# Optimization experiments

Hardware: AMD Instinct MI355X
Metric: run time of the kernel (lower is better)

Reference implementation:

```python
import jax, jax.numpy as jnp
import numpy as np

N_HEADS = 32
N_KV_HEADS = 8
HEAD_DIM = 64
D_MODEL = 2048
SLIDING_WINDOW = 512
ROPE_THETA = 10000.0
PAST_LENGTH = 0
EPS = 1e-6


def setup_inputs() -> dict:
    key = jax.random.key(0)
    k1, k2, k3 = jax.random.split(key, 3)
    B, S = 1, 2048
    q_size = N_HEADS * HEAD_DIM
    kv_size = N_KV_HEADS * HEAD_DIM
    return {
        "x": jax.random.normal(k1, (B, S, D_MODEL), dtype=jnp.float32),
        "w_qkv": jax.random.normal(k2, (q_size + 2 * kv_size, D_MODEL), dtype=jnp.float32) * (D_MODEL ** -0.5),
        "w_out": jax.random.normal(k3, (D_MODEL, q_size), dtype=jnp.float32) * (q_size ** -0.5),
        "q_norm_w": jnp.ones((HEAD_DIM,), dtype=jnp.float32),
        "k_norm_w": jnp.ones((HEAD_DIM,), dtype=jnp.float32),
    }


def _rms_norm(x, w):
    xf = x.astype(jnp.float32)
    rms = jax.lax.rsqrt(jnp.mean(xf * xf, axis=-1, keepdims=True) + EPS)
    return (xf * rms).astype(x.dtype) * w


def _rope(q, k, past_length):
    # q: [b, h, s, d], k: [b, kv, s, d]
    s, d = q.shape[2], q.shape[3]
    inv_freq = 1.0 / (ROPE_THETA ** (jnp.arange(0, d, 2, dtype=jnp.float32) / d))
    pos = jnp.arange(s, dtype=jnp.float32) + past_length
    ang = pos[:, None] * inv_freq[None, :]            # [s, d/2]
    emb = jnp.concatenate([ang, ang], axis=-1)        # [s, d]
    cos, sin = jnp.cos(emb), jnp.sin(emb)

    def rot_half(x):
        x1, x2 = jnp.split(x, 2, axis=-1)
        return jnp.concatenate([-x2, x1], axis=-1)

    q = q * cos + rot_half(q) * sin
    k = k * cos + rot_half(k) * sin
    return q, k


def _sliding_mask(seq_len, total_len, past_length):
    q_idx = jnp.arange(seq_len)[:, None]
    k_idx = jnp.arange(total_len)[None, :]
    causal = (q_idx + past_length) >= k_idx
    window = (q_idx + past_length - k_idx) < SLIDING_WINDOW
    keep = causal & window
    return jnp.where(keep, 0.0, -jnp.inf).astype(jnp.float32)[None, None]


def reference(x, w_qkv, w_out, q_norm_w, k_norm_w):
    b, s, _ = x.shape
    n_rep = N_HEADS // N_KV_HEADS
    q_size = N_HEADS * HEAD_DIM
    kv_size = N_KV_HEADS * HEAD_DIM

    qkv = jnp.einsum('bsd,od->bso', x, w_qkv)
    q, k, v = jnp.split(qkv, [q_size, q_size + kv_size], axis=-1)
    q = q.reshape(b, s, N_HEADS, HEAD_DIM).transpose(0, 2, 1, 3)
    k = k.reshape(b, s, N_KV_HEADS, HEAD_DIM).transpose(0, 2, 1, 3)
    v = v.reshape(b, s, N_KV_HEADS, HEAD_DIM).transpose(0, 2, 1, 3)

    q = _rms_norm(q, q_norm_w)
    k = _rms_norm(k, k_norm_w)
    q, k = _rope(q, k, PAST_LENGTH)

    k_rep = jnp.repeat(k, n_rep, axis=1)  # [b, H, s, d]
    v_rep = jnp.repeat(v, n_rep, axis=1)

    scale = HEAD_DIM ** -0.5
    scores = jnp.einsum('bhqd,bhkd->bhqk', q, k_rep) * scale
    scores = scores + _sliding_mask(s, s, PAST_LENGTH)
    probs = jax.nn.softmax(scores, axis=-1)
    attn = jnp.einsum('bhqk,bhkd->bhqd', probs, v_rep)

    attn = attn.transpose(0, 2, 1, 3).reshape(b, s, q_size)
    return jnp.einsum('bso,do->bsd', attn, w_out)
```

## Files before the change

### kernel.cpp

```cpp
#include <hip/hip_runtime.h>

typedef unsigned short u16;
typedef unsigned int u32;
typedef __bf16 bf16x8 __attribute__((ext_vector_type(8)));
typedef float f32x4 __attribute__((ext_vector_type(4)));
typedef float f32x16 __attribute__((ext_vector_type(16)));
typedef u16 u16x8 __attribute__((ext_vector_type(8)));
typedef u32 u32x2 __attribute__((ext_vector_type(2)));
typedef u32 u32x4 __attribute__((ext_vector_type(4)));

#define MFMA16(a, b, c) __builtin_amdgcn_mfma_f32_16x16x32_bf16((a), (b), (c), 0, 0, 0)
#define MFMA32(a, b, c) __builtin_amdgcn_mfma_f32_32x32x16_bf16((a), (b), (c), 0, 0, 0)

__device__ __forceinline__ u16 f2bf(float f) {
    unsigned int u = __float_as_uint(f);
    u = (u + 0x7FFF + ((u >> 16) & 1)) >> 16;
    return (u16)u;
}

__device__ __forceinline__ u32 cvtpk(float a, float b) {
    u32 d;
    asm("v_cvt_pk_bf16_f32 %0, %1, %2" : "=v"(d) : "v"(a), "v"(b));
    return d;
}

__device__ __forceinline__ void gld_lds16(const u16* g, u16* l) {
    __builtin_amdgcn_global_load_lds(
        (const __attribute__((address_space(1))) unsigned int*)g,
        (__attribute__((address_space(3))) unsigned int*)l, 16, 0, 0);
}

__global__ __launch_bounds__(256) void cvt_bf16(const float* __restrict__ in,
                                                u16* __restrict__ out, int n4) {
    int idx = blockIdx.x * blockDim.x + threadIdx.x;
    int stride = gridDim.x * blockDim.x;
    for (int i = idx; i < n4; i += stride) {
        float4 v = reinterpret_cast<const float4*>(in)[i];
        ushort4 o;
        o.x = f2bf(v.x); o.y = f2bf(v.y); o.z = f2bf(v.z); o.w = f2bf(v.w);
        reinterpret_cast<ushort4*>(out)[i] = o;
    }
}

__global__ __launch_bounds__(256) void reduce_add(const float4* __restrict__ a,
                                                  const float4* __restrict__ b,
                                                  float4* __restrict__ o, int n4) {
    int idx = blockIdx.x * blockDim.x + threadIdx.x;
    int stride = gridDim.x * blockDim.x;
    for (int i = idx; i < n4; i += stride) {
        float4 va = a[i], vb = b[i];
        float4 vo = {va.x + vb.x, va.y + vb.y, va.z + vb.z, va.w + vb.w};
        o[i] = vo;
    }
}

template <int SPLITK, int RM, int RN, int XN>
__global__ __launch_bounds__(256) void gemm_bt(const u16* __restrict__ A,
                                               const u16* __restrict__ B,
                                               float* __restrict__ C,
                                               int M, int N, int K) {
    __shared__ __align__(16) u16 As[3][128 * 32];
    __shared__ __align__(16) u16 Bs[3][128 * 32];

    int bid = blockIdx.x;
    int xcd = bid & 7;
    int r = bid >> 3;
    int tm = (xcd / XN) * RM + (r / RN);
    int tn = (xcd % XN) * RN + (r % RN);
    int m0 = tm << 7, n0 = tn << 7;

    int Ks = K / SPLITK;
    int kbase = blockIdx.y * Ks;
    float* Cs = C + (size_t)blockIdx.y * ((size_t)M * N);

    int t = threadIdx.x;
    int w = t >> 6, l = t & 63, lrow = l & 15, lhi = l >> 4;
    int wr = w >> 1, wc = w & 1;

    int e0 = t * 8;
    int row0 = t >> 2;
    int col0 = (((t & 3) ^ ((t >> 3) & 3)) << 3);

    const u16* Ag = A + (size_t)m0 * K + kbase;
    const u16* Bg = B + (size_t)n0 * K + kbase;

    auto stage = [&](int sbuf, int kt) {
        int k0 = kt << 5;
        gld_lds16(Ag + (size_t)row0 * K + k0 + col0, &As[sbuf][e0]);
        gld_lds16(Ag + (size_t)(row0 + 64) * K + k0 + col0, &As[sbuf][e0 + 2048]);
        gld_lds16(Bg + (size_t)row0 * K + k0 + col0, &Bs[sbuf][e0]);
        gld_lds16(Bg + (size_t)(row0 + 64) * K + k0 + col0, &Bs[sbuf][e0 + 2048]);
    };

    f32x4 acc[4][4] = {};
    int NT = Ks >> 5;
    stage(0, 0); stage(1, 1); stage(2, 2);
    asm volatile("s_waitcnt vmcnt(8)" ::: "memory");
    asm volatile("s_barrier" ::: "memory");
    int cur = 0;
    for (int kt = 0; kt < NT; ++kt) {
        bf16x8 af[4], bfr[4];
#pragma unroll
        for (int i = 0; i < 4; ++i) {
            int row = wr * 64 + i * 16 + lrow;
            af[i] = *(const bf16x8*)&As[cur][row * 32 + ((lhi ^ ((row >> 1) & 3)) << 3)];
        }
#pragma unroll
        for (int j = 0; j < 4; ++j) {
            int row = wc * 64 + j * 16 + lrow;
            bfr[j] = *(const bf16x8*)&Bs[cur][row * 32 + ((lhi ^ ((row >> 1) & 3)) << 3)];
        }
        asm volatile("s_waitcnt lgkmcnt(0)" ::: "memory");
        __builtin_amdgcn_sched_barrier(0);
        asm volatile("s_barrier" ::: "memory");
        if (kt + 3 < NT) stage(cur, kt + 3);
#pragma unroll
        for (int i = 0; i < 4; ++i)
#pragma unroll
            for (int j = 0; j < 4; ++j)
                acc[i][j] = MFMA16(af[i], bfr[j], acc[i][j]);
        if (kt + 1 < NT) {
            if (kt + 3 < NT)      asm volatile("s_waitcnt vmcnt(8)" ::: "memory");
            else if (kt + 2 < NT) asm volatile("s_waitcnt vmcnt(4)" ::: "memory");
            else                  asm volatile("s_waitcnt vmcnt(0)" ::: "memory");
            asm volatile("s_barrier" ::: "memory");
        }
        cur = (cur == 2) ? 0 : cur + 1;
    }
#pragma unroll
    for (int i = 0; i < 4; ++i) {
#pragma unroll
        for (int j = 0; j < 4; ++j) {
            int crow = m0 + wr * 64 + i * 16 + lhi * 4;
            int ccol = n0 + wc * 64 + j * 16 + lrow;
            float* cp = Cs + (size_t)crow * N + ccol;
#pragma unroll
            for (int r2 = 0; r2 < 4; ++r2) cp[(size_t)r2 * N] = acc[i][j][r2];
        }
    }
}

__global__ __launch_bounds__(256) void qkv_post(const float* __restrict__ qkv0,
                                                const float* __restrict__ qkv1,
                                                const float* __restrict__ qw,
                                                const float* __restrict__ kw,
                                                u16* __restrict__ qb,
                                                u16* __restrict__ kb,
                                                u16* __restrict__ vb) {
    const float C = 0.18033688011112042f;
    int s = blockIdx.x;
    int t = threadIdx.x, w = t >> 6, lane = t & 63;
    const float* row0 = qkv0 + (size_t)s * 3072;
    const float* row1 = qkv1 + (size_t)s * 3072;
    int d2 = lane & 31;
    float inv = exp2f(-(float)d2 * (13.287712379549449f / 32.0f));
    float ang = (float)s * inv;
    float cs = cosf(ang), sn = sinf(ang);
    for (int h = w; h < 48; h += 4) {
        float v = row0[h * 64 + lane] + row1[h * 64 + lane];
        if (h < 40) {
            float ss = v * v;
#pragma unroll
            for (int m = 32; m; m >>= 1) ss += __shfl_xor(ss, m);
            float rms = rsqrtf(ss * (1.0f / 64.0f) + 1e-6f);
            float wgt = (h < 32) ? qw[lane] : kw[lane];
            v = v * rms * wgt;
            float part = __shfl_xor(v, 32);
            float rot = (lane < 32) ? -part : part;
            v = v * cs + rot * sn;
            if (h < 32)
                qb[((size_t)h * 2048 + s) * 64 + lane] = f2bf(v * C);
            else
                kb[((size_t)(h - 32) * 2048 + s) * 64 + lane] = f2bf(v);
        } else {
            vb[((size_t)(h - 40) * 2048 + s) * 64 + lane] = f2bf(v);
        }
    }
}

__global__ __launch_bounds__(256) void transpose_v(const u16* __restrict__ vb,
                                                   u16* __restrict__ vt) {
    int kv = blockIdx.y;
    int s0 = blockIdx.x * 256;
    __shared__ __align__(16) u16 tile[64][256];
    int t = threadIdx.x;
    int sl = t >> 3;
    int d0 = (t & 7) * 8;
#pragma unroll
    for (int j = 0; j < 8; ++j) {
        int s = sl + j * 32;
        u16x8 v = *(const u16x8*)(vb + ((size_t)kv * 2048 + s0 + s) * 64 + d0);
#pragma unroll
        for (int e = 0; e < 8; ++e) tile[d0 + e][s] = v[e];
    }
    __syncthreads();
    int d = t >> 2;
    int so = (t & 3) * 64;
#pragma unroll
    for (int j = 0; j < 8; ++j) {
        int s_local = so + j * 8;
        *(u16x8*)(vt + ((size_t)kv * 64 + d) * 2048 + s0 + s_local) =
            *(const u16x8*)&tile[d][s_local];
    }
}

__global__ __launch_bounds__(256) void attn_fa7(const u16* __restrict__ qb,
                                                const u16* __restrict__ kb,
                                                const u16* __restrict__ vt,
                                                u16* __restrict__ ab) {
    int qt = blockIdx.x, h = blockIdx.y, kv = h >> 2;
    int t = threadIdx.x, w = t >> 6, l = t & 63;
    int lq = l & 31, hi = l >> 5;
    int qlo_blk = qt * 128;
    int qlo = qlo_blk + w * 32;
    __shared__ __align__(16) u16 Kt[2][32 * 64];
    __shared__ __align__(16) u16 Vt[2][64 * 32];
    __shared__ u16 sm[4][32][66];

    const u16* qrow = qb + ((size_t)h * 2048 + qlo + lq) * 64 + hi * 8;
    bf16x8 qf[4];
#pragma unroll
    for (int dk = 0; dk < 4; ++dk) qf[dk] = *(const bf16x8*)(qrow + dk * 16);

    f32x16 oa = {}, ob = {};
    float lsum = 0.f;

    int ktA = (qlo_blk >= 512) ? ((qlo_blk >> 5) - 16) : 0;
    int ktB = (qlo_blk >> 5) + 3;
    const u16* kb_h = kb + (size_t)kv * 2048 * 64;
    const u16* vt_h = vt + (size_t)kv * 64 * 2048;

    int sk_row = t >> 3, sk_c = ((t & 7) ^ (sk_row & 7)) << 3;
    int sv_row = t >> 2, sv_c = (((t & 3) ^ ((t >> 3) & 3))) << 3;

    auto stage = [&](int buf, int kt) {
        int k0 = kt << 5;
        gld_lds16(kb_h + (size_t)(k0 + sk_row) * 64 + sk_c, &Kt[buf][t * 8]);
        gld_lds16(vt_h + (size_t)sv_row * 2048 + k0 + sv_c, &Vt[buf][t * 8]);
    };

    stage(0, ktA);
    int cur = 0;
    for (int kt = ktA; kt <= ktB; ++kt) {
        if (kt < ktB) {
            stage(cur ^ 1, kt + 1);
            asm volatile("s_waitcnt vmcnt(2)" ::: "memory");
        } else {
            asm volatile("s_waitcnt vmcnt(0)" ::: "memory");
        }
        asm volatile("s_barrier" ::: "memory");

        int k0 = kt << 5;
        bool active = (k0 <= qlo + 31) && (k0 >= qlo - 542);
        if (active) {
            bf16x8 kf[4], vaf[2], vbf[2];
#pragma unroll
            for (int c = 0; c < 4; ++c)
                kf[c] = *(const bf16x8*)&Kt[cur][lq * 64 + (((c * 2 + hi) ^ (lq & 7)) << 3)];
#pragma unroll
            for (int vi = 0; vi < 2; ++vi) {
                int swz = ((vi * 2 + hi) ^ ((lq >> 1) & 3)) << 3;
                vaf[vi] = *(const bf16x8*)&Vt[cur][lq * 32 + swz];
                vbf[vi] = *(const bf16x8*)&Vt[cur][(lq + 32) * 32 + swz];
            }
            asm volatile("s_waitcnt lgkmcnt(0)" ::: "memory");
            __builtin_amdgcn_sched_barrier(0);

            f32x16 s = {};
            s = MFMA32(kf[0], qf[0], s);
            s = MFMA32(kf[1], qf[1], s);
            s = MFMA32(kf[2], qf[2], s);
            s = MFMA32(kf[3], qf[3], s);

            bool edge = (k0 + 31 > qlo) || (qlo + 31 - k0 >= 512);
            if (edge) {
                int q = qlo + lq;
#pragma unroll
                for (int r = 0; r < 16; ++r) {
                    int k = k0 + (r & 3) + 8 * (r >> 2) + 4 * hi;
                    if (!((unsigned)(q - k) < 512u)) s[r] = -1e30f;
                }
            }
            float p[16];
#pragma unroll
            for (int r = 0; r < 16; ++r) {
                p[r] = exp2f(s[r]);
                lsum += p[r];
            }
            u32 pk0 = cvtpk(p[0], p[1]),   pk1 = cvtpk(p[2], p[3]);
            u32 pk2 = cvtpk(p[4], p[5]),   pk3 = cvtpk(p[6], p[7]);
            u32 pk4 = cvtpk(p[8], p[9]),   pk5 = cvtpk(p[10], p[11]);
            u32 pk6 = cvtpk(p[12], p[13]), pk7 = cvtpk(p[14], p[15]);
            u32x2 r02 = __builtin_amdgcn_permlane32_swap(pk0, pk2, false, false);
            u32x2 r13 = __builtin_amdgcn_permlane32_swap(pk1, pk3, false, false);
            u32x2 r46 = __builtin_amdgcn_permlane32_swap(pk4, pk6, false, false);
            u32x2 r57 = __builtin_amdgcn_permlane32_swap(pk5, pk7, false, false);
            bf16x8 b0, b1;
            {
                u32* bp = (u32*)&b0;
                bp[0] = r02[0]; bp[1] = r13[0]; bp[2] = r02[1]; bp[3] = r13[1];
                u32* bq = (u32*)&b1;
                bq[0] = r46[0]; bq[1] = r57[0]; bq[2] = r46[1]; bq[3] = r57[1];
            }
            oa = MFMA32(vaf[0], b0, oa);
            oa = MFMA32(vaf[1], b1, oa);
            ob = MFMA32(vbf[0], b0, ob);
            ob = MFMA32(vbf[1], b1, ob);
        }
        asm volatile("s_barrier" ::: "memory");
        cur ^= 1;
    }

    lsum += __shfl_xor(lsum, 32);
    float inv = 1.0f / lsum;
#pragma unroll
    for (int rp = 0; rp < 8; ++rp) {
        int r = rp * 2;
        int d = (r & 3) + 8 * (r >> 2) + 4 * hi;
        *(u32*)&sm[w][lq][d]      = cvtpk(oa[r] * inv, oa[r + 1] * inv);
        *(u32*)&sm[w][lq][d + 32] = cvtpk(ob[r] * inv, ob[r + 1] * inv);
    }
    asm volatile("s_waitcnt lgkmcnt(0)" ::: "memory");
    int qr = l >> 1, dbase = (l & 1) * 32;
    size_t orow = (size_t)(qlo + qr) * 2048 + h * 64 + dbase;
#pragma unroll
    for (int c2 = 0; c2 < 8; ++c2) {
        u32 w0 = *(const u32*)&sm[w][qr][dbase + c2 * 4];
        u32 w1 = *(const u32*)&sm[w][qr][dbase + c2 * 4 + 2];
        u32x2 val = { w0, w1 };
        *(u32x2*)(ab + orow + c2 * 4) = val;
    }
}

extern "C" void kernel_launch(void* const* d_in, const int* in_sizes, int n_in,
                              void* d_out, int out_size, void* d_ws, size_t ws_size,
                              hipStream_t stream) {
    const float* x     = (const float*)d_in[0];
    const float* w_qkv = (const float*)d_in[1];
    const float* w_out = (const float*)d_in[2];
    const float* qw    = (const float*)d_in[3];
    const float* kw    = (const float*)d_in[4];
    float* out = (float*)d_out;

    char* ws = (char*)d_ws;
    u16*   x_b    = (u16*)(ws);
    u16*   wB     = (u16*)(ws + 8388608);
    u16*   q_b    = (u16*)(ws);
    u16*   k_b    = (u16*)(ws + 8388608);
    u16*   v_b    = (u16*)(ws + 10485760);
    u16*   v_t    = (u16*)(ws + 12582912);
    float* P0     = (float*)(ws + 20971520);
    float* O0     = (float*)(ws + 20971520);
    float* O1     = (float*)(ws + 37748736);
    u16*   attn_b = (u16*)(ws + 54525952);

    cvt_bf16<<<2048, 256, 0, stream>>>(x, x_b, 2048 * 2048 / 4);
    cvt_bf16<<<2048, 256, 0, stream>>>(w_qkv, wB, 3072 * 2048 / 4);
    gemm_bt<2, 8, 6, 4><<<dim3(384, 2), 256, 0, stream>>>(x_b, wB, P0, 2048, 3072, 2048);
    qkv_post<<<2048, 256, 0, stream>>>(P0, P0 + (size_t)2048 * 3072, qw, kw, q_b, k_b, v_b);
    transpose_v<<<dim3(8, 8), 256, 0, stream>>>(v_b, v_t);
    attn_fa7<<<dim3(16, 32), 256, 0, stream>>>(q_b, k_b, v_t, attn_b);
    cvt_bf16<<<2048, 256, 0, stream>>>(w_out, wB, 2048 * 2048 / 4);
    gemm_bt<2, 4, 8, 2><<<dim3(256, 2), 256, 0, stream>>>(attn_b, wB, O0, 2048, 2048, 2048);
    reduce_add<<<1024, 256, 0, stream>>>((const float4*)O0, (const float4*)O1,
                                         (float4*)out, 2048 * 2048 / 4);
}
```

Measured before the change: 140.8 us.

## Store QKV split-K partials as bf16 and drop split-K on output projection

The QKV GEMM now writes its two split-K partial results as bf16 instead of fp32, halving the intermediate traffic that qkv_post reads. The output projection no longer uses split-K: it runs with a single K slice straight into the output buffer, which removes the fp32 partial buffers and the reduce_add kernel. The trade-offs are extra rounding error in the QKV partials and only 256 blocks for the output GEMM, each doing a full-length K loop, which may under-occupy the GPU.

```diff
diff --git a/kernel.cpp b/kernel.cpp
--- a/kernel.cpp
+++ b/kernel.cpp
@@ -16,6 +16,10 @@
     unsigned int u = __float_as_uint(f);
     u = (u + 0x7FFF + ((u >> 16) & 1)) >> 16;
     return (u16)u;
+}
+
+__device__ __forceinline__ float bf2f(u16 v) {
+    return __uint_as_float(((u32)v) << 16);
 }
 
 __device__ __forceinline__ u32 cvtpk(float a, float b) {
@@ -42,22 +46,10 @@
     }
 }
 
-__global__ __launch_bounds__(256) void reduce_add(const float4* __restrict__ a,
-                                                  const float4* __restrict__ b,
-                                                  float4* __restrict__ o, int n4) {
-    int idx = blockIdx.x * blockDim.x + threadIdx.x;
-    int stride = gridDim.x * blockDim.x;
-    for (int i = idx; i < n4; i += stride) {
-        float4 va = a[i], vb = b[i];
-        float4 vo = {va.x + vb.x, va.y + vb.y, va.z + vb.z, va.w + vb.w};
-        o[i] = vo;
-    }
-}
-
-template <int SPLITK, int RM, int RN, int XN>
+template <int SPLITK, int RM, int RN, int XN, bool OBF16>
 __global__ __launch_bounds__(256) void gemm_bt(const u16* __restrict__ A,
                                                const u16* __restrict__ B,
-                                               float* __restrict__ C,
+                                               void* __restrict__ Cv,
                                                int M, int N, int K) {
     __shared__ __align__(16) u16 As[3][128 * 32];
     __shared__ __align__(16) u16 Bs[3][128 * 32];
@@ -71,7 +63,6 @@
 
     int Ks = K / SPLITK;
     int kbase = blockIdx.y * Ks;
-    float* Cs = C + (size_t)blockIdx.y * ((size_t)M * N);
 
     int t = threadIdx.x;
     int w = t >> 6, l = t & 63, lrow = l & 15, lhi = l >> 4;
@@ -133,15 +124,23 @@
         for (int j = 0; j < 4; ++j) {
             int crow = m0 + wr * 64 + i * 16 + lhi * 4;
             int ccol = n0 + wc * 64 + j * 16 + lrow;
-            float* cp = Cs + (size_t)crow * N + ccol;
-#pragma unroll
-            for (int r2 = 0; r2 < 4; ++r2) cp[(size_t)r2 * N] = acc[i][j][r2];
-        }
-    }
-}
-
-__global__ __launch_bounds__(256) void qkv_post(const float* __restrict__ qkv0,
-                                                const float* __restrict__ qkv1,
+            if (OBF16) {
+                u16* cp = (u16*)Cv + (size_t)blockIdx.y * ((size_t)M * N)
+                                   + (size_t)crow * N + ccol;
+#pragma unroll
+                for (int r2 = 0; r2 < 4; ++r2) cp[(size_t)r2 * N] = f2bf(acc[i][j][r2]);
+            } else {
+                float* cp = (float*)Cv + (size_t)blockIdx.y * ((size_t)M * N)
+                                       + (size_t)crow * N + ccol;
+#pragma unroll
+                for (int r2 = 0; r2 < 4; ++r2) cp[(size_t)r2 * N] = acc[i][j][r2];
+            }
+        }
+    }
+}
+
+__global__ __launch_bounds__(256) void qkv_post(const u16* __restrict__ qkv0,
+                                                const u16* __restrict__ qkv1,
                                                 const float* __restrict__ qw,
                                                 const float* __restrict__ kw,
                                                 u16* __restrict__ qb,
@@ -150,14 +149,14 @@
     const float C = 0.18033688011112042f;
     int s = blockIdx.x;
     int t = threadIdx.x, w = t >> 6, lane = t & 63;
-    const float* row0 = qkv0 + (size_t)s * 3072;
-    const float* row1 = qkv1 + (size_t)s * 3072;
+    const u16* row0 = qkv0 + (size_t)s * 3072;
+    const u16* row1 = qkv1 + (size_t)s * 3072;
     int d2 = lane & 31;
     float inv = exp2f(-(float)d2 * (13.287712379549449f / 32.0f));
     float ang = (float)s * inv;
     float cs = cosf(ang), sn = sinf(ang);
     for (int h = w; h < 48; h += 4) {
-        float v = row0[h * 64 + lane] + row1[h * 64 + lane];
+        float v = bf2f(row0[h * 64 + lane]) + bf2f(row1[h * 64 + lane]);
         if (h < 40) {
             float ss = v * v;
 #pragma unroll
@@ -349,19 +348,18 @@
     u16*   k_b    = (u16*)(ws + 8388608);
     u16*   v_b    = (u16*)(ws + 10485760);
     u16*   v_t    = (u16*)(ws + 12582912);
-    float* P0     = (float*)(ws + 20971520);
-    float* O0     = (float*)(ws + 20971520);
-    float* O1     = (float*)(ws + 37748736);
+    u16*   P0     = (u16*)(ws + 20971520);
     u16*   attn_b = (u16*)(ws + 54525952);
 
     cvt_bf16<<<2048, 256, 0, stream>>>(x, x_b, 2048 * 2048 / 4);
     cvt_bf16<<<2048, 256, 0, stream>>>(w_qkv, wB, 3072 * 2048 / 4);
-    gemm_bt<2, 8, 6, 4><<<dim3(384, 2), 256, 0, stream>>>(x_b, wB, P0, 2048, 3072, 2048);
-    qkv_post<<<2048, 256, 0, stream>>>(P0, P0 + (size_t)2048 * 3072, qw, kw, q_b, k_b, v_b);
+    gemm_bt<2, 8, 6, 4, true><<<dim3(384, 2), 256, 0, stream>>>(
+        x_b, wB, P0, 2048, 3072, 2048);
+    qkv_post<<<2048, 256, 0, stream>>>(P0, P0 + (size_t)2048 * 3072, qw, kw,
+                                       q_b, k_b, v_b);
     transpose_v<<<dim3(8, 8), 256, 0, stream>>>(v_b, v_t);
     attn_fa7<<<dim3(16, 32), 256, 0, stream>>>(q_b, k_b, v_t, attn_b);
     cvt_bf16<<<2048, 256, 0, stream>>>(w_out, wB, 2048 * 2048 / 4);
-    gemm_bt<2, 4, 8, 2><<<dim3(256, 2), 256, 0, stream>>>(attn_b, wB, O0, 2048, 2048, 2048);
-    reduce_add<<<1024, 256, 0, stream>>>((const float4*)O0, (const float4*)O1,
-                                         (float4*)out, 2048 * 2048 / 4);
-}
+    gemm_bt<1, 4, 8, 2, false><<<dim3(256, 1), 256, 0, stream>>>(
+        attn_b, wB, out, 2048, 2048, 2048);
+}
```

Result: no change. 141.0 us (+0.2%).
